# Kernel optimization log

Hardware: AMD Instinct MI355X
Metric: run time of the kernel (lower is better)

## Reference

```python
import math
import jax, jax.numpy as jnp
import numpy as np

D, DK, DV = 256, 256, 256

def setup_inputs() -> dict:
    key = jax.random.key(0)
    ks = jax.random.split(key, 7)
    s = 1.0 / math.sqrt(D)
    return {
        "x": jax.random.normal(ks[0], (4, 4096, D), dtype=jnp.float32),
        "Wq": jax.random.uniform(ks[1], (D, DK), jnp.float32, -s, s),
        "bq": jax.random.uniform(ks[2], (DK,), jnp.float32, -s, s),
        "Wk": jax.random.uniform(ks[3], (D, DK), jnp.float32, -s, s),
        "bk": jax.random.uniform(ks[4], (DK,), jnp.float32, -s, s),
        "Wv": jax.random.uniform(ks[5], (D, DV), jnp.float32, -s, s),
        "bv": jax.random.uniform(ks[6], (DV,), jnp.float32, -s, s),
    }

def reference(x, Wq, bq, Wk, bk, Wv, bv):
    # x: [B, S, D]
    q = x @ Wq + bq            # [B, S, DK]
    k = x @ Wk + bk            # [B, S, DK]
    v = x @ Wv + bv            # [B, S, DV]
    scores = jnp.einsum('bqd,bkd->bqk', q, k) / math.sqrt(DK)  # [B, S, S]
    S = x.shape[1]
    causal = jnp.tril(jnp.ones((S, S), dtype=bool))  # True = keep
    scores = jnp.where(causal, scores, -jnp.inf)
    attn = jax.nn.softmax(scores, axis=-1)
    return jnp.einsum('bqk,bkd->bqd', attn, v)  # [B, S, DV]
```

## Files before the change

### kernel.cpp

```cpp
#include <hip/hip_runtime.h>
#include <cmath>

#define LOG2E 1.4426950408889634f

typedef __attribute__((ext_vector_type(8))) __bf16 bf16x8;
typedef __attribute__((ext_vector_type(4))) float f32x4;
typedef __attribute__((ext_vector_type(16))) float f32x16;
typedef __attribute__((ext_vector_type(4))) float float4v;
typedef __attribute__((ext_vector_type(4))) unsigned int uint4v;
typedef __attribute__((ext_vector_type(8))) unsigned short ushort8v;
typedef __attribute__((ext_vector_type(2))) int int2v;

__device__ __forceinline__ unsigned short f2bf(float f) {
  unsigned int u = __builtin_bit_cast(unsigned int, f);
  u += 0x7fffu + ((u >> 16) & 1u);
  return (unsigned short)(u >> 16);
}

__device__ __forceinline__ unsigned int cvtpk(float lo, float hi) {
  unsigned int r;
  asm volatile("v_cvt_pk_bf16_f32 %0, %1, %2" : "=v"(r) : "v"(lo), "v"(hi));
  return r;
}

__device__ __forceinline__ void gload_lds16(const unsigned short* g, unsigned short* l) {
  __builtin_amdgcn_global_load_lds(
      (const __attribute__((address_space(1))) unsigned int*)(const void*)g,
      (__attribute__((address_space(3))) unsigned int*)(void*)l, 16, 0, 0);
}

__global__ __launch_bounds__(256) void prep_w_kernel(
    const float* __restrict__ Wq, const float* __restrict__ Wk,
    const float* __restrict__ Wv, unsigned short* __restrict__ Wt) {
  const int w = blockIdx.y, n = blockIdx.x, k = threadIdx.x;
  const float* W = (w == 0) ? Wq : ((w == 1) ? Wk : Wv);
  const float s = (w == 0) ? (LOG2E / 16.0f) : 1.0f;
  Wt[w * 65536 + n * 256 + k] = f2bf(W[k * 256 + n] * s);
}

__global__ __launch_bounds__(256) void proj_kernel(
    const float* __restrict__ x, const unsigned short* __restrict__ Wt,
    const float* __restrict__ bq, const float* __restrict__ bk,
    const float* __restrict__ bv,
    unsigned short* __restrict__ q_o, unsigned short* __restrict__ k_o,
    unsigned short* __restrict__ vt_o) {
  __shared__ unsigned short vlds[128 * 72];

  const int mt = blockIdx.x;
  const int nfh = blockIdx.y;
  const int tid = threadIdx.x;
  const int wid = tid >> 6, lane = tid & 63, g = (lane >> 4) & 3, c = lane & 15;
  const int row_base = mt * 64 + wid * 16;

  bf16x8 a[8];
  const float* xr = x + (size_t)(row_base + c) * 256;
#pragma unroll
  for (int s = 0; s < 8; ++s) {
    const float4v v0 = *(const float4v*)(xr + s * 32 + g * 8);
    const float4v v1 = *(const float4v*)(xr + s * 32 + g * 8 + 4);
    union { bf16x8 v; unsigned short u[8]; } t;
#pragma unroll
    for (int j = 0; j < 4; ++j) { t.u[j] = f2bf(v0[j]); t.u[4 + j] = f2bf(v1[j]); }
    a[s] = t.v;
  }

  const unsigned short* w0 = Wt;
  const unsigned short* w1 = Wt + 65536;
  const unsigned short* w2 = Wt + 131072;

#pragma unroll
  for (int nfi = 0; nfi < 8; ++nfi) {
    const int nf = nfh * 8 + nfi;
    f32x4 aq = (f32x4){0.f, 0.f, 0.f, 0.f};
    f32x4 ak = (f32x4){0.f, 0.f, 0.f, 0.f};
    f32x4 av = (f32x4){0.f, 0.f, 0.f, 0.f};
    const unsigned short* r0 = w0 + (size_t)(nf * 16 + c) * 256;
    const unsigned short* r1 = w1 + (size_t)(nf * 16 + c) * 256;
    const unsigned short* r2 = w2 + (size_t)(nf * 16 + c) * 256;
#pragma unroll
    for (int s = 0; s < 8; ++s) {
      bf16x8 b0 = *(const bf16x8*)(r0 + s * 32 + g * 8);
      bf16x8 b1 = *(const bf16x8*)(r1 + s * 32 + g * 8);
      bf16x8 b2 = *(const bf16x8*)(r2 + s * 32 + g * 8);
      aq = __builtin_amdgcn_mfma_f32_16x16x32_bf16(a[s], b0, aq, 0, 0, 0);
      ak = __builtin_amdgcn_mfma_f32_16x16x32_bf16(a[s], b1, ak, 0, 0, 0);
      av = __builtin_amdgcn_mfma_f32_16x16x32_bf16(a[s], b2, av, 0, 0, 0);
    }
    const float bql = bq[nf * 16 + c] * (LOG2E / 16.0f);
    const float bkl = bk[nf * 16 + c];
    const float bvl = bv[nf * 16 + c];
#pragma unroll
    for (int r = 0; r < 4; ++r) {
      const int row = row_base + g * 4 + r;
      q_o[(size_t)row * 256 + nf * 16 + c] = f2bf(aq[r] + bql);
      k_o[(size_t)row * 256 + nf * 16 + c] = f2bf(ak[r] + bkl);
      vlds[(nfi * 16 + c) * 72 + (wid * 16 + g * 4 + r)] = f2bf(av[r] + bvl);
    }
  }

  __syncthreads();

  const int bb = mt >> 6;
  const int s0 = (mt & 63) * 64;
  unsigned short* vout = vt_o + ((size_t)bb * 256 + nfh * 128) * 4096 + s0;
#pragma unroll
  for (int it = 0; it < 4; ++it) {
    const int idx = it * 256 + tid;
    const int dl = idx >> 3, s8 = idx & 7;
    ushort8v val = *(const ushort8v*)(vlds + dl * 72 + s8 * 8);
    *(ushort8v*)(vout + (size_t)dl * 4096 + s8 * 8) = val;
  }
}

__global__ __launch_bounds__(256, 2) void attn_kernel(
    const unsigned short* __restrict__ qg, const unsigned short* __restrict__ kg,
    const unsigned short* __restrict__ vtg, float* __restrict__ out) {
  __shared__ unsigned short Klds[64 * 256];
  __shared__ unsigned short Vlds[256 * 64];
  __shared__ float llds[2][32];

  const int tid = threadIdx.x;
  const int wid = tid >> 6, lane = tid & 63;
  const int hi = lane >> 5, q5 = lane & 31;
  const int wk = wid & 1, dh = wid >> 1;
  const int bid = blockIdx.x;
  const int half = bid >> 8, c = bid & 255, b = c & 3;
  const int qt = half ? (c >> 2) : (127 - (c >> 2));
  const int T = (qt >> 1) + 1;

  const unsigned short* qb = qg + (size_t)b * 4096 * 256;
  const unsigned short* kb = kg + (size_t)b * 4096 * 256;
  const unsigned short* vb = vtg + (size_t)b * 256 * 4096;
  float* outb = out + (size_t)b * 4096 * 256;

  const int qrow = qt * 32 + q5;

  int koff[8], voff[8];
#pragma unroll
  for (int i = 0; i < 8; ++i) {
    const int kr = wid * 16 + i * 2 + (lane >> 5);
    const int c8 = (lane & 31) ^ (kr & 7);
    koff[i] = kr * 256 + c8 * 8;
    const int d = wid * 64 + i * 8 + (lane >> 3);
    const int c8v = (lane & 7) ^ (d & 7);
    voff[i] = d * 4096 + c8v * 8;
  }

  auto stage = [&](int t) {
    const unsigned short* kp = kb + (size_t)t * 16384;
    const unsigned short* vp = vb + t * 64;
#pragma unroll
    for (int i = 0; i < 8; ++i)
      gload_lds16(kp + koff[i], &Klds[(wid * 8 + i) * 512]);
#pragma unroll
    for (int i = 0; i < 8; ++i)
      gload_lds16(vp + voff[i], &Vlds[(wid * 8 + i) * 512]);
  };

  bf16x8 bqf[16];
  {
    const unsigned short* qr = qb + (size_t)qrow * 256;
#pragma unroll
    for (int s = 0; s < 16; ++s) bqf[s] = *(const bf16x8*)(qr + s * 16 + hi * 8);
  }

  float l = 0.f;
  f32x16 o[4];
#pragma unroll
  for (int d = 0; d < 4; ++d)
#pragma unroll
    for (int r = 0; r < 16; ++r) o[d][r] = 0.f;

  const int krow = wk * 32 + q5;
  const int ksw = (krow & 7) << 3;
  const int kbase = krow * 256;

  int kcolr[16];
#pragma unroll
  for (int r = 0; r < 16; ++r) kcolr[r] = wk * 32 + (r & 3) + 8 * (r >> 2) + 4 * hi;

  stage(0);
  for (int t = 0; t < T; ++t) {
    __syncthreads();

    f32x16 sa, sb;
#pragma unroll
    for (int r = 0; r < 16; ++r) { sa[r] = 0.f; sb[r] = 0.f; }
#pragma unroll
    for (int s = 0; s < 8; ++s) {
      bf16x8 ka0 = *(const bf16x8*)(&Klds[(kbase + s * 16 + hi * 8) ^ ksw]);
      bf16x8 ka1 = *(const bf16x8*)(&Klds[(kbase + (s + 8) * 16 + hi * 8) ^ ksw]);
      sa = __builtin_amdgcn_mfma_f32_32x32x16_bf16(ka0, bqf[s], sa, 0, 0, 0);
      sb = __builtin_amdgcn_mfma_f32_32x32x16_bf16(ka1, bqf[s + 8], sb, 0, 0, 0);
    }
    f32x16 sc = sa + sb;

    if (t == T - 1) {
#pragma unroll
      for (int r = 0; r < 16; ++r)
        if (t * 64 + kcolr[r] > qrow) sc[r] = -1e30f;
    }

    float p[16];
#pragma unroll
    for (int r = 0; r < 16; ++r) p[r] = __builtin_amdgcn_exp2f(sc[r]);
    {
      float s0 = (p[0] + p[1]) + (p[2] + p[3]);
      float s1 = (p[4] + p[5]) + (p[6] + p[7]);
      float s2 = (p[8] + p[9]) + (p[10] + p[11]);
      float s3 = (p[12] + p[13]) + (p[14] + p[15]);
      l += (s0 + s1) + (s2 + s3);
    }

    bf16x8 pfrag[2];
#pragma unroll
    for (int s2 = 0; s2 < 2; ++s2) {
      const int base = s2 * 8;
      unsigned int X = cvtpk(p[base + 0], p[base + 1]);
      unsigned int Y = cvtpk(p[base + 2], p[base + 3]);
      unsigned int Z = cvtpk(p[base + 4], p[base + 5]);
      unsigned int W = cvtpk(p[base + 6], p[base + 7]);
#if __has_builtin(__builtin_amdgcn_permlane32_swap)
      int2v rx = __builtin_amdgcn_permlane32_swap((int)X, (int)Z, false, false);
      int2v ry = __builtin_amdgcn_permlane32_swap((int)Y, (int)W, false, false);
      uint4v u = (uint4v){(unsigned)rx[0], (unsigned)ry[0], (unsigned)rx[1], (unsigned)ry[1]};
#else
      const unsigned int Xp = __shfl_xor((int)X, 32);
      const unsigned int Yp = __shfl_xor((int)Y, 32);
      const unsigned int Zp = __shfl_xor((int)Z, 32);
      const unsigned int Wp = __shfl_xor((int)W, 32);
      uint4v u = (uint4v){hi ? Zp : X, hi ? Wp : Y, hi ? Z : Xp, hi ? W : Yp};
#endif
      pfrag[s2] = __builtin_bit_cast(bf16x8, u);
    }

#pragma unroll
    for (int dblk = 0; dblk < 4; ++dblk) {
      const int drow = (dh * 4 + dblk) * 32 + q5;
      const int vsw = (drow & 7) << 3;
      const int vbase = drow * 64 + wk * 32;
#pragma unroll
      for (int s2 = 0; s2 < 2; ++s2) {
        bf16x8 va = *(const bf16x8*)(&Vlds[(vbase + s2 * 16 + hi * 8) ^ vsw]);
        o[dblk] = __builtin_amdgcn_mfma_f32_32x32x16_bf16(va, pfrag[s2], o[dblk], 0, 0, 0);
      }
    }

    if (t + 1 < T) {
      __syncthreads();
      stage(t + 1);
    }
  }

  l += __shfl_xor(l, 32);
  if (dh == 0 && hi == 0) llds[wk][q5] = l;
  __syncthreads();
  const float L = llds[0][q5] + llds[1][q5];
  const float scale = 1.0f / L;

  float* oz = (float*)Klds;
  if (wk == 1) {
#pragma unroll
    for (int dblk = 0; dblk < 4; ++dblk)
#pragma unroll
      for (int r = 0; r < 16; ++r) {
        const int dg = (dh * 4 + dblk) * 32 + (r & 3) + 8 * (r >> 2) + 4 * hi;
        oz[dg * 32 + q5] = o[dblk][r];
      }
  }
  __syncthreads();
  if (wk == 0) {
#pragma unroll
    for (int dblk = 0; dblk < 4; ++dblk) {
#pragma unroll
      for (int q2 = 0; q2 < 4; ++q2) {
        float4v val;
#pragma unroll
        for (int e = 0; e < 4; ++e) {
          const int r = q2 * 4 + e;
          const int dg = (dh * 4 + dblk) * 32 + e + 8 * q2 + 4 * hi;
          val[e] = (o[dblk][r] + oz[dg * 32 + q5]) * scale;
        }
        *(float4v*)(outb + (size_t)qrow * 256 + (dh * 4 + dblk) * 32 + 8 * q2 + 4 * hi) = val;
      }
    }
  }
}

extern "C" void kernel_launch(void* const* d_in, const int* in_sizes, int n_in,
                              void* d_out, int out_size, void* d_ws, size_t ws_size,
                              hipStream_t stream) {
  (void)in_sizes; (void)n_in; (void)out_size; (void)ws_size;
  const float* x  = (const float*)d_in[0];
  const float* Wq = (const float*)d_in[1];
  const float* bq = (const float*)d_in[2];
  const float* Wk = (const float*)d_in[3];
  const float* bk = (const float*)d_in[4];
  const float* Wv = (const float*)d_in[5];
  const float* bv = (const float*)d_in[6];
  float* out = (float*)d_out;

  unsigned short* qs  = (unsigned short*)d_ws;
  unsigned short* ks  = qs  + (size_t)16384 * 256;
  unsigned short* vts = ks  + (size_t)16384 * 256;
  unsigned short* Wt  = vts + (size_t)16384 * 256;

  prep_w_kernel<<<dim3(256, 3), 256, 0, stream>>>(Wq, Wk, Wv, Wt);
  proj_kernel<<<dim3(256, 2), 256, 0, stream>>>(x, Wt, bq, bk, bv, qs, ks, vts);
  attn_kernel<<<512, 256, 0, stream>>>(qs, ks, vts, out);
}
```

Baseline: 166.9 us.

## Split causal KV range across two warp groups per block; tile weight transpose

The attention kernel now runs 512 threads per block as two 4-wave groups. Each group processes half of the causal KV tiles using its own K/V LDS buffers, and the partial outputs and row sums are merged through LDS at the end. The goal is to shorten each block's serial KV loop and raise the number of waves resident per CU. In exchange it doubles LDS per block, which may limit how many blocks fit on a CU, and adds an extra reduction phase. The weight-prep kernel also switches to an LDS-tiled transpose with vector loads and stores, replacing the strided per-element transpose.

```diff
diff --git a/kernel.cpp b/kernel.cpp
--- a/kernel.cpp
+++ b/kernel.cpp
@@ -32,10 +32,32 @@
 __global__ __launch_bounds__(256) void prep_w_kernel(
     const float* __restrict__ Wq, const float* __restrict__ Wk,
     const float* __restrict__ Wv, unsigned short* __restrict__ Wt) {
-  const int w = blockIdx.y, n = blockIdx.x, k = threadIdx.x;
+  __shared__ float lds[64 * 65];
+
+  const int w = blockIdx.y;
+  const int kt = blockIdx.x & 3, nt = blockIdx.x >> 2;
   const float* W = (w == 0) ? Wq : ((w == 1) ? Wk : Wv);
   const float s = (w == 0) ? (LOG2E / 16.0f) : 1.0f;
-  Wt[w * 65536 + n * 256 + k] = f2bf(W[k * 256 + n] * s);
+  const int t = threadIdx.x;
+
+#pragma unroll
+  for (int it = 0; it < 4; ++it) {
+    const int idx = it * 256 + t;
+    const int r = idx >> 4, c4 = (idx & 15) * 4;
+    const float4v v = *(const float4v*)(W + (size_t)(kt * 64 + r) * 256 + nt * 64 + c4);
+#pragma unroll
+    for (int j = 0; j < 4; ++j) lds[(c4 + j) * 65 + r] = v[j];
+  }
+  __syncthreads();
+#pragma unroll
+  for (int it = 0; it < 2; ++it) {
+    const int idx = it * 256 + t;
+    const int rn = idx >> 3, c8 = (idx & 7) * 8;
+    ushort8v o;
+#pragma unroll
+    for (int j = 0; j < 8; ++j) o[j] = f2bf(lds[rn * 65 + c8 + j] * s);
+    *(ushort8v*)(Wt + w * 65536 + (size_t)(nt * 64 + rn) * 256 + kt * 64 + c8) = o;
+  }
 }
 
 __global__ __launch_bounds__(256) void proj_kernel(
@@ -112,21 +134,24 @@
   }
 }
 
-__global__ __launch_bounds__(256, 2) void attn_kernel(
+__global__ __launch_bounds__(512, 2) void attn_kernel(
     const unsigned short* __restrict__ qg, const unsigned short* __restrict__ kg,
     const unsigned short* __restrict__ vtg, float* __restrict__ out) {
-  __shared__ unsigned short Klds[64 * 256];
-  __shared__ unsigned short Vlds[256 * 64];
-  __shared__ float llds[2][32];
+  __shared__ unsigned short Klds[2][64 * 256];
+  __shared__ unsigned short Vlds[2][256 * 64];
+  __shared__ float llds[2][2][32];
 
   const int tid = threadIdx.x;
   const int wid = tid >> 6, lane = tid & 63;
   const int hi = lane >> 5, q5 = lane & 31;
-  const int wk = wid & 1, dh = wid >> 1;
+  const int g = wid >> 2, dh = (wid >> 1) & 1, wk = wid & 1, wg = wid & 3;
   const int bid = blockIdx.x;
-  const int half = bid >> 8, c = bid & 255, b = c & 3;
-  const int qt = half ? (c >> 2) : (127 - (c >> 2));
+  const int half = bid >> 8, k6 = (bid >> 2) & 63, b = bid & 3;
+  const int qt = half ? k6 : 127 - k6;
   const int T = (qt >> 1) + 1;
+  const int S1 = (T + 1) >> 1;
+  const int tb = g ? S1 : 0;
+  const int te = g ? T : S1;
 
   const unsigned short* qb = qg + (size_t)b * 4096 * 256;
   const unsigned short* kb = kg + (size_t)b * 4096 * 256;
@@ -138,10 +163,10 @@
   int koff[8], voff[8];
 #pragma unroll
   for (int i = 0; i < 8; ++i) {
-    const int kr = wid * 16 + i * 2 + (lane >> 5);
+    const int kr = wg * 16 + i * 2 + (lane >> 5);
     const int c8 = (lane & 31) ^ (kr & 7);
     koff[i] = kr * 256 + c8 * 8;
-    const int d = wid * 64 + i * 8 + (lane >> 3);
+    const int d = wg * 64 + i * 8 + (lane >> 3);
     const int c8v = (lane & 7) ^ (d & 7);
     voff[i] = d * 4096 + c8v * 8;
   }
@@ -151,10 +176,10 @@
     const unsigned short* vp = vb + t * 64;
 #pragma unroll
     for (int i = 0; i < 8; ++i)
-      gload_lds16(kp + koff[i], &Klds[(wid * 8 + i) * 512]);
+      gload_lds16(kp + koff[i], &Klds[g][(wg * 8 + i) * 512]);
 #pragma unroll
     for (int i = 0; i < 8; ++i)
-      gload_lds16(vp + voff[i], &Vlds[(wid * 8 + i) * 512]);
+      gload_lds16(vp + voff[i], &Vlds[g][(wg * 8 + i) * 512]);
   };
 
   bf16x8 bqf[16];
@@ -179,97 +204,113 @@
 #pragma unroll
   for (int r = 0; r < 16; ++r) kcolr[r] = wk * 32 + (r & 3) + 8 * (r >> 2) + 4 * hi;
 
-  stage(0);
-  for (int t = 0; t < T; ++t) {
+  if (tb < te) stage(tb);
+
+  for (int st = 0; st < S1; ++st) {
+    const int t = tb + st;
+    const bool act = t < te;
     __syncthreads();
 
-    f32x16 sa, sb;
-#pragma unroll
-    for (int r = 0; r < 16; ++r) { sa[r] = 0.f; sb[r] = 0.f; }
-#pragma unroll
-    for (int s = 0; s < 8; ++s) {
-      bf16x8 ka0 = *(const bf16x8*)(&Klds[(kbase + s * 16 + hi * 8) ^ ksw]);
-      bf16x8 ka1 = *(const bf16x8*)(&Klds[(kbase + (s + 8) * 16 + hi * 8) ^ ksw]);
-      sa = __builtin_amdgcn_mfma_f32_32x32x16_bf16(ka0, bqf[s], sa, 0, 0, 0);
-      sb = __builtin_amdgcn_mfma_f32_32x32x16_bf16(ka1, bqf[s + 8], sb, 0, 0, 0);
+    if (act) {
+      f32x16 sa, sb;
+#pragma unroll
+      for (int r = 0; r < 16; ++r) { sa[r] = 0.f; sb[r] = 0.f; }
+#pragma unroll
+      for (int s = 0; s < 8; ++s) {
+        bf16x8 ka0 = *(const bf16x8*)(&Klds[g][(kbase + s * 16 + hi * 8) ^ ksw]);
+        bf16x8 ka1 = *(const bf16x8*)(&Klds[g][(kbase + (s + 8) * 16 + hi * 8) ^ ksw]);
+        sa = __builtin_amdgcn_mfma_f32_32x32x16_bf16(ka0, bqf[s], sa, 0, 0, 0);
+        sb = __builtin_amdgcn_mfma_f32_32x32x16_bf16(ka1, bqf[s + 8], sb, 0, 0, 0);
+      }
+      f32x16 sc = sa + sb;
+
+      if (t == T - 1) {
+#pragma unroll
+        for (int r = 0; r < 16; ++r)
+          if (t * 64 + kcolr[r] > qrow) sc[r] = -1e30f;
+      }
+
+      float p[16];
+#pragma unroll
+      for (int r = 0; r < 16; ++r) p[r] = __builtin_amdgcn_exp2f(sc[r]);
+      {
+        float s0 = (p[0] + p[1]) + (p[2] + p[3]);
+        float s1 = (p[4] + p[5]) + (p[6] + p[7]);
+        float s2 = (p[8] + p[9]) + (p[10] + p[11]);
+        float s3 = (p[12] + p[13]) + (p[14] + p[15]);
+        l += (s0 + s1) + (s2 + s3);
+      }
+
+      bf16x8 pfrag[2];
+#pragma unroll
+      for (int s2 = 0; s2 < 2; ++s2) {
+        const int base = s2 * 8;
+        unsigned int X = cvtpk(p[base + 0], p[base + 1]);
+        unsigned int Y = cvtpk(p[base + 2], p[base + 3]);
+        unsigned int Z = cvtpk(p[base + 4], p[base + 5]);
+        unsigned int W = cvtpk(p[base + 6], p[base + 7]);
+#if __has_builtin(__builtin_amdgcn_permlane32_swap)
+        int2v rx = __builtin_amdgcn_permlane32_swap((int)X, (int)Z, false, false);
+        int2v ry = __builtin_amdgcn_permlane32_swap((int)Y, (int)W, false, false);
+        uint4v u = (uint4v){(unsigned)rx[0], (unsigned)ry[0], (unsigned)rx[1], (unsigned)ry[1]};
+#else
+        const unsigned int Xp = __shfl_xor((int)X, 32);
+        const unsigned int Yp = __shfl_xor((int)Y, 32);
+        const unsigned int Zp = __shfl_xor((int)Z, 32);
+        const unsigned int Wp = __shfl_xor((int)W, 32);
+        uint4v u = (uint4v){hi ? Zp : X, hi ? Wp : Y, hi ? Z : Xp, hi ? W : Yp};
+#endif
+        pfrag[s2] = __builtin_bit_cast(bf16x8, u);
+      }
+
+#pragma unroll
+      for (int dblk = 0; dblk < 4; ++dblk) {
+        const int drow = (dh * 4 + dblk) * 32 + q5;
+        const int vsw = (drow & 7) << 3;
+        const int vbase = drow * 64 + wk * 32;
+#pragma unroll
+        for (int s2 = 0; s2 < 2; ++s2) {
+          bf16x8 va = *(const bf16x8*)(&Vlds[g][(vbase + s2 * 16 + hi * 8) ^ vsw]);
+          o[dblk] = __builtin_amdgcn_mfma_f32_32x32x16_bf16(va, pfrag[s2], o[dblk], 0, 0, 0);
+        }
+      }
     }
-    f32x16 sc = sa + sb;
-
-    if (t == T - 1) {
-#pragma unroll
-      for (int r = 0; r < 16; ++r)
-        if (t * 64 + kcolr[r] > qrow) sc[r] = -1e30f;
-    }
-
-    float p[16];
-#pragma unroll
-    for (int r = 0; r < 16; ++r) p[r] = __builtin_amdgcn_exp2f(sc[r]);
-    {
-      float s0 = (p[0] + p[1]) + (p[2] + p[3]);
-      float s1 = (p[4] + p[5]) + (p[6] + p[7]);
-      float s2 = (p[8] + p[9]) + (p[10] + p[11]);
-      float s3 = (p[12] + p[13]) + (p[14] + p[15]);
-      l += (s0 + s1) + (s2 + s3);
-    }
-
-    bf16x8 pfrag[2];
-#pragma unroll
-    for (int s2 = 0; s2 < 2; ++s2) {
-      const int base = s2 * 8;
-      unsigned int X = cvtpk(p[base + 0], p[base + 1]);
-      unsigned int Y = cvtpk(p[base + 2], p[base + 3]);
-      unsigned int Z = cvtpk(p[base + 4], p[base + 5]);
-      unsigned int W = cvtpk(p[base + 6], p[base + 7]);
-#if __has_builtin(__builtin_amdgcn_permlane32_swap)
-      int2v rx = __builtin_amdgcn_permlane32_swap((int)X, (int)Z, false, false);
-      int2v ry = __builtin_amdgcn_permlane32_swap((int)Y, (int)W, false, false);
-      uint4v u = (uint4v){(unsigned)rx[0], (unsigned)ry[0], (unsigned)rx[1], (unsigned)ry[1]};
-#else
-      const unsigned int Xp = __shfl_xor((int)X, 32);
-      const unsigned int Yp = __shfl_xor((int)Y, 32);
-      const unsigned int Zp = __shfl_xor((int)Z, 32);
-      const unsigned int Wp = __shfl_xor((int)W, 32);
-      uint4v u = (uint4v){hi ? Zp : X, hi ? Wp : Y, hi ? Z : Xp, hi ? W : Yp};
-#endif
-      pfrag[s2] = __builtin_bit_cast(bf16x8, u);
-    }
-
-#pragma unroll
-    for (int dblk = 0; dblk < 4; ++dblk) {
-      const int drow = (dh * 4 + dblk) * 32 + q5;
-      const int vsw = (drow & 7) << 3;
-      const int vbase = drow * 64 + wk * 32;
-#pragma unroll
-      for (int s2 = 0; s2 < 2; ++s2) {
-        bf16x8 va = *(const bf16x8*)(&Vlds[(vbase + s2 * 16 + hi * 8) ^ vsw]);
-        o[dblk] = __builtin_amdgcn_mfma_f32_32x32x16_bf16(va, pfrag[s2], o[dblk], 0, 0, 0);
-      }
-    }
-
-    if (t + 1 < T) {
-      __syncthreads();
-      stage(t + 1);
-    }
+
+    __syncthreads();
+    if (t + 1 < te) stage(t + 1);
   }
 
   l += __shfl_xor(l, 32);
-  if (dh == 0 && hi == 0) llds[wk][q5] = l;
-  __syncthreads();
-  const float L = llds[0][q5] + llds[1][q5];
+  if (hi == 0 && dh == 0) llds[g][wk][q5] = l;
+  __syncthreads();
+  const float L = llds[0][0][q5] + llds[0][1][q5] + llds[1][0][q5] + llds[1][1][q5];
   const float scale = 1.0f / L;
 
-  float* oz = (float*)Klds;
+  float* oz0 = (float*)&Klds[0][0];
+  float* oz1 = (float*)&Klds[1][0];
+  float* ozg = g ? oz1 : oz0;
+
   if (wk == 1) {
 #pragma unroll
     for (int dblk = 0; dblk < 4; ++dblk)
 #pragma unroll
       for (int r = 0; r < 16; ++r) {
         const int dg = (dh * 4 + dblk) * 32 + (r & 3) + 8 * (r >> 2) + 4 * hi;
-        oz[dg * 32 + q5] = o[dblk][r];
-      }
-  }
-  __syncthreads();
-  if (wk == 0) {
+        ozg[dg * 32 + q5] = o[dblk][r];
+      }
+  }
+  __syncthreads();
+  if (wk == 0 && g == 1) {
+#pragma unroll
+    for (int dblk = 0; dblk < 4; ++dblk)
+#pragma unroll
+      for (int r = 0; r < 16; ++r) {
+        const int dg = (dh * 4 + dblk) * 32 + (r & 3) + 8 * (r >> 2) + 4 * hi;
+        oz1[dg * 32 + q5] += o[dblk][r];
+      }
+  }
+  __syncthreads();
+  if (wk == 0 && g == 0) {
 #pragma unroll
     for (int dblk = 0; dblk < 4; ++dblk) {
 #pragma unroll
@@ -279,7 +320,7 @@
         for (int e = 0; e < 4; ++e) {
           const int r = q2 * 4 + e;
           const int dg = (dh * 4 + dblk) * 32 + e + 8 * q2 + 4 * hi;
-          val[e] = (o[dblk][r] + oz[dg * 32 + q5]) * scale;
+          val[e] = (o[dblk][r] + oz0[dg * 32 + q5] + oz1[dg * 32 + q5]) * scale;
         }
         *(float4v*)(outb + (size_t)qrow * 256 + (dh * 4 + dblk) * 32 + 8 * q2 + 4 * hi) = val;
       }
@@ -305,7 +346,7 @@
   unsigned short* vts = ks  + (size_t)16384 * 256;
   unsigned short* Wt  = vts + (size_t)16384 * 256;
 
-  prep_w_kernel<<<dim3(256, 3), 256, 0, stream>>>(Wq, Wk, Wv, Wt);
+  prep_w_kernel<<<dim3(16, 3), 256, 0, stream>>>(Wq, Wk, Wv, Wt);
   proj_kernel<<<dim3(256, 2), 256, 0, stream>>>(x, Wt, bq, bk, bv, qs, ks, vts);
-  attn_kernel<<<512, 256, 0, stream>>>(qs, ks, vts, out);
-}
+  attn_kernel<<<512, 512, 0, stream>>>(qs, ks, vts, out);
+}
```

New measurement: 168.9 us. No clear change (+1.2%).
